# Kernel tuning notes

Measured on AMD Instinct MI355X. Metric: run time of the kernel, lower is better.

## Reference

```python
import jax, jax.numpy as jnp
import numpy as np

ALPHA = 0.2        # LeakyReLU negative slope (self.alpha)
NEG = -9e15        # mask value used by the torch module


def gru_cell(x, h, W_ih, W_hh, b_ih, b_hh):
    """torch.nn.GRUCell math. x, h: [N, F]; W_*: [3F, F]; b_*: [3F]. Gate order r,z,n."""
    gi = x @ W_ih.T + b_ih
    gh = h @ W_hh.T + b_hh
    ir, iz, i_n = jnp.split(gi, 3, axis=-1)
    hr, hz, h_n = jnp.split(gh, 3, axis=-1)
    r = jax.nn.sigmoid(ir + hr)
    z = jax.nn.sigmoid(iz + hz)
    n = jnp.tanh(i_n + r * h_n)
    return (1.0 - z) * n + z * h


def setup_inputs() -> dict:
    key = jax.random.key(0)
    N, F = 8192, 256
    ks = jax.random.split(key, 8)
    inputs = jax.random.normal(ks[0], (N, F), jnp.float32)
    # GRUCell parameters
    W_ih = jax.random.normal(ks[1], (3 * F, F), jnp.float32) / np.sqrt(F)
    W_hh = jax.random.normal(ks[2], (3 * F, F), jnp.float32) / np.sqrt(F)
    b_ih = jax.random.normal(ks[3], (3 * F,), jnp.float32) * 0.01
    b_hh = jax.random.normal(ks[4], (3 * F,), jnp.float32) * 0.01
    # GAT attention vector a: [2F, 1]
    a = jax.random.normal(ks[5], (2 * F, 1), jnp.float32) / np.sqrt(2.0 * F)
    # per-node neighbor pair (encodes weight_dict's 1-/2-neighbor cases)
    nbr = jax.random.randint(ks[6], (N, 2), 0, N)
    # dense adjacency, values in {0,1}
    adj = jax.random.randint(ks[7], (N, N), 0, 2).astype(jnp.int32)
    return dict(inputs=inputs, W_ih=W_ih, W_hh=W_hh, b_ih=b_ih, b_hh=b_hh,
                a=a, nbr=nbr, adj=adj)


def reference(inputs, W_ih, W_hh, b_ih, b_hh, a, nbr, adj):
    F_dim = inputs.shape[1]
    # per-node GRU aggregation: hidden = neighbor1 feature, input = neighbor2 feature
    h = inputs[nbr[:, 0]]                      # [N, F]
    x = inputs[nbr[:, 1]]                      # [N, F]
    outs = gru_cell(x, h, W_ih, W_hh, b_ih, b_hh)  # [N, F]
    # GAT scores: e[i,j] = leakyrelu([outs_i || outs_j] . a) = leakyrelu(f1_i + f2_j)
    # (decomposed -- avoids materializing the [N*N, 2F] concat of the original)
    a1 = a[:F_dim, 0]                          # [F]
    a2 = a[F_dim:, 0]                          # [F]
    e = jax.nn.leaky_relu((outs @ a1)[:, None] + (outs @ a2)[None, :], ALPHA)  # [N, N]
    e = jnp.where(adj > 0, e, NEG)
    return jax.nn.softmax(e, axis=1)
```

## Files before the change

### kernel.cpp

```cpp
#include <hip/hip_runtime.h>
#include <hip/hip_bf16.h>

#define NN 8192
#define FF 256
#define NEGV -9000000000000000.0f

typedef __bf16 bf16x8 __attribute__((ext_vector_type(8)));
typedef float f32x4 __attribute__((ext_vector_type(4)));
typedef int i32x4 __attribute__((ext_vector_type(4)));

__device__ __forceinline__ void load_lds16(const void* g, void* l) {
  auto gp = (const __attribute__((address_space(1))) void*)(uintptr_t)g;
  auto lp = (__attribute__((address_space(3))) void*)(uint32_t)(uintptr_t)l;
  __builtin_amdgcn_global_load_lds(gp, lp, 16, 0, 0);
}

__global__ __launch_bounds__(256) void k_convert(const float* __restrict__ inputs,
                                                 const float* __restrict__ Wih,
                                                 const float* __restrict__ Whh,
                                                 __hip_bfloat16* __restrict__ ibf,
                                                 __hip_bfloat16* __restrict__ Wc) {
  const int gid = blockIdx.x * 256 + threadIdx.x;
  const float* src;
  __hip_bfloat16* dst;
  if (gid < 262144) {
    src = inputs + (size_t)gid * 8;
    dst = ibf + (size_t)gid * 8;
  } else {
    const int o = gid - 262144;
    const int l = o & 63;
    const int ks = (o >> 6) & 7;
    const int w = (o >> 9) & 3;
    const int fbb = (o >> 11) & 3;
    const int g = o >> 13;
    const int row = g * 256 + fbb * 64 + w * 16 + (l & 15);
    const int col = (l >> 4) * 8 + ks * 32;
    src = (row < 768) ? (Wih + (size_t)row * FF + col)
                      : (Whh + (size_t)(row - 768) * FF + col);
    dst = Wc + (size_t)o * 8;
  }
  const float4 v0 = *(const float4*)src;
  const float4 v1 = *(const float4*)(src + 4);
  union { __hip_bfloat16 h[8]; uint4 u; } t;
  t.h[0] = __float2bfloat16(v0.x); t.h[1] = __float2bfloat16(v0.y);
  t.h[2] = __float2bfloat16(v0.z); t.h[3] = __float2bfloat16(v0.w);
  t.h[4] = __float2bfloat16(v1.x); t.h[5] = __float2bfloat16(v1.y);
  t.h[6] = __float2bfloat16(v1.z); t.h[7] = __float2bfloat16(v1.w);
  *(uint4*)dst = t.u;
}

__global__ __launch_bounds__(256) void k_gru(const __hip_bfloat16* __restrict__ ibf,
                                             const __hip_bfloat16* __restrict__ Wpk,
                                             const float* __restrict__ inputs,
                                             const int* __restrict__ nbr,
                                             const float* __restrict__ b_ih,
                                             const float* __restrict__ b_hh,
                                             const float* __restrict__ a,
                                             float* __restrict__ p1a,
                                             float* __restrict__ p2a) {
  __shared__ __align__(16) __hip_bfloat16 Ax[16 * 256];
  __shared__ __align__(16) __hip_bfloat16 Ah[16 * 256];
  __shared__ int hrow_s[16];
  __shared__ float r1[4][16], r2[4][16];
  const int rb = blockIdx.x * 16;
  const int fb = blockIdx.y;
  const int tid = threadIdx.x;
  const int w = tid >> 6, l = tid & 63;
  const int fl = l & 15, q = l >> 4;

  if (tid < 16) hrow_s[tid] = nbr[2 * (rb + tid)];

#pragma unroll
  for (int j = 0; j < 2; ++j) {
    const int r = w * 4 + j * 2 + (l >> 5);
    const int cs = l & 31;
    const int gc = cs ^ (r & 7);
    const int xr = nbr[2 * (rb + r) + 1];
    const int hr_ = nbr[2 * (rb + r)];
    load_lds16((const char*)(ibf + (size_t)xr * FF) + gc * 16,
               (char*)Ax + (w * 4 + j * 2) * 512);
    load_lds16((const char*)(ibf + (size_t)hr_ * FF) + gc * 16,
               (char*)Ah + (w * 4 + j * 2) * 512);
  }
  __syncthreads();

  const int f = fb * 64 + w * 16 + fl;
  const float bir = b_ih[f], biz = b_ih[256 + f], bin_ = b_ih[512 + f];
  const float bhr = b_hh[f], bhz = b_hh[256 + f], bhn = b_hh[512 + f];
  const float a1f = a[f], a2f = a[256 + f];

  f32x4 acc[6];
#pragma unroll
  for (int g = 0; g < 6; ++g) acc[g] = (f32x4){0, 0, 0, 0};

  bf16x8 axf[8], ahf[8];
#pragma unroll
  for (int ks = 0; ks < 8; ++ks) {
    const int c = ks * 4 + q;
    axf[ks] = *(const bf16x8*)((const char*)Ax + fl * 512 + (c ^ (fl & 7)) * 16);
    ahf[ks] = *(const bf16x8*)((const char*)Ah + fl * 512 + (c ^ (fl & 7)) * 16);
  }
#pragma unroll
  for (int g = 0; g < 3; ++g) {
    const int bi = ((g * 16 + fb * 4 + w) * 8) * 64 + l;
    const int bh = (((3 + g) * 16 + fb * 4 + w) * 8) * 64 + l;
#pragma unroll
    for (int ks = 0; ks < 8; ++ks) {
      const bf16x8 bfi = *(const bf16x8*)(Wpk + (size_t)(bi + ks * 64) * 8);
      const bf16x8 bfh = *(const bf16x8*)(Wpk + (size_t)(bh + ks * 64) * 8);
      acc[g]     = __builtin_amdgcn_mfma_f32_16x16x32_bf16(axf[ks], bfi, acc[g], 0, 0, 0);
      acc[3 + g] = __builtin_amdgcn_mfma_f32_16x16x32_bf16(ahf[ks], bfh, acc[3 + g], 0, 0, 0);
    }
  }

  float p1[4], p2[4];
#pragma unroll
  for (int j = 0; j < 4; ++j) {
    const int row = q * 4 + j;
    const float ir = acc[0][j] + bir;
    const float iz = acc[1][j] + biz;
    const float in_ = acc[2][j] + bin_;
    const float hrv = acc[3][j] + bhr;
    const float hzv = acc[4][j] + bhz;
    const float hnv = acc[5][j] + bhn;
    const float r_ = 1.f / (1.f + __expf(-(ir + hrv)));
    const float z_ = 1.f / (1.f + __expf(-(iz + hzv)));
    const float n_ = tanhf(in_ + r_ * hnv);
    const float hval = inputs[(size_t)hrow_s[row] * FF + f];
    const float o = (1.f - z_) * n_ + z_ * hval;
    p1[j] = o * a1f;
    p2[j] = o * a2f;
  }

#pragma unroll
  for (int j = 0; j < 4; ++j) {
#pragma unroll
    for (int off = 1; off < 16; off <<= 1) {
      p1[j] += __shfl_xor(p1[j], off);
      p2[j] += __shfl_xor(p2[j], off);
    }
  }
  if (fl == 0) {
#pragma unroll
    for (int j = 0; j < 4; ++j) {
      r1[w][q * 4 + j] = p1[j];
      r2[w][q * 4 + j] = p2[j];
    }
  }
  __syncthreads();
  if (tid < 16) {
    p1a[fb * NN + rb + tid] = r1[0][tid] + r1[1][tid] + r1[2][tid] + r1[3][tid];
  } else if (tid < 32) {
    const int t2 = tid - 16;
    p2a[fb * NN + rb + t2] = r2[0][t2] + r2[1][t2] + r2[2][t2] + r2[3][t2];
  }
}

__global__ __launch_bounds__(256) void k_reduce(const float* __restrict__ p1a,
                                                const float* __restrict__ p2a,
                                                float* __restrict__ s1,
                                                float* __restrict__ s2) {
  const int i = blockIdx.x * 256 + threadIdx.x;
  s1[i] = p1a[i] + p1a[NN + i] + p1a[2 * NN + i] + p1a[3 * NN + i];
  s2[i] = p2a[i] + p2a[NN + i] + p2a[2 * NN + i] + p2a[3 * NN + i];
}

__global__ __launch_bounds__(256, 5) void k_softmax(const int* __restrict__ adj,
                                                    const float* __restrict__ s1,
                                                    const float* __restrict__ s2,
                                                    float* __restrict__ out) {
  __shared__ float red[4];
  const int row = blockIdx.x;
  const int t = threadIdx.x;
  const i32x4* adjv = (const i32x4*)(adj + (size_t)row * NN);
  i32x4 a4[8];
#pragma unroll
  for (int k = 0; k < 8; ++k) a4[k] = __builtin_nontemporal_load(adjv + k * 256 + t);
  f32x4 sv[8];
#pragma unroll
  for (int k = 0; k < 8; ++k) sv[k] = *(const f32x4*)(s2 + (k * 256 + t) * 4);
  const float s1v = s1[row];

  float tsum = 0.f;
#pragma unroll
  for (int k = 0; k < 8; ++k) {
#pragma unroll
    for (int c = 0; c < 4; ++c) {
      float x = s1v + sv[k][c];
      x = (x > 0.f) ? x : 0.2f * x;
      x = (a4[k][c] > 0) ? x : NEGV;
      tsum += __expf(x);
    }
  }
#pragma unroll
  for (int off = 32; off; off >>= 1) tsum += __shfl_xor(tsum, off);
  if ((t & 63) == 0) red[t >> 6] = tsum;
  __syncthreads();
  const float inv = 1.f / (red[0] + red[1] + red[2] + red[3]);
  float* orow = out + (size_t)row * NN;
#pragma unroll
  for (int k = 0; k < 8; ++k) {
    const int v = k * 256 + t;
    f32x4 o;
#pragma unroll
    for (int c = 0; c < 4; ++c) {
      float x = s1v + sv[k][c];
      x = (x > 0.f) ? x : 0.2f * x;
      x = (a4[k][c] > 0) ? x : NEGV;
      o[c] = __expf(x) * inv;
    }
    __builtin_nontemporal_store(o, (f32x4*)(orow + v * 4));
  }
}

extern "C" void kernel_launch(void* const* d_in, const int* in_sizes, int n_in,
                              void* d_out, int out_size, void* d_ws, size_t ws_size,
                              hipStream_t stream) {
  const float* inputs = (const float*)d_in[0];
  const float* W_ih   = (const float*)d_in[1];
  const float* W_hh   = (const float*)d_in[2];
  const float* b_ih   = (const float*)d_in[3];
  const float* b_hh   = (const float*)d_in[4];
  const float* a      = (const float*)d_in[5];
  const int*   nbr    = (const int*)d_in[6];
  const int*   adj    = (const int*)d_in[7];
  float* out = (float*)d_out;

  __hip_bfloat16* ibf = (__hip_bfloat16*)((char*)d_out + (64u << 20));
  __hip_bfloat16* Wpk = (__hip_bfloat16*)((char*)d_out + (80u << 20));
  float* p1a = (float*)((char*)d_out + (96u << 20));
  float* p2a = p1a + 4 * NN;
  float* s1 = (float*)d_ws;
  float* s2 = s1 + NN;

  k_convert<<<1216, 256, 0, stream>>>(inputs, W_ih, W_hh, ibf, Wpk);
  k_gru<<<dim3(512, 4), 256, 0, stream>>>(ibf, Wpk, inputs, nbr, b_ih, b_hh, a, p1a, p2a);
  k_reduce<<<32, 256, 0, stream>>>(p1a, p2a, s1, s2);
  k_softmax<<<NN, 256, 0, stream>>>(adj, s1, s2, out);
}
```

Baseline: 123.3 us.

## Process eight softmax rows per block with double-buffered adjacency prefetch

The softmax kernel now handles eight consecutive rows per block instead of one. The s2 vector is loaded once per block and reused across those rows. The next row's adjacency is prefetched into registers while the current row is reduced and written, so load latency overlaps with compute. The cost is higher register pressure (two sets of adjacency registers, and the occupancy hint is removed) and a grid of 1024 blocks, which may leave fewer waves per CU to hide memory latency.

```diff
diff --git a/kernel.cpp b/kernel.cpp
--- a/kernel.cpp
+++ b/kernel.cpp
@@ -165,51 +165,62 @@
   s2[i] = p2a[i] + p2a[NN + i] + p2a[2 * NN + i] + p2a[3 * NN + i];
 }
 
-__global__ __launch_bounds__(256, 5) void k_softmax(const int* __restrict__ adj,
-                                                    const float* __restrict__ s1,
-                                                    const float* __restrict__ s2,
-                                                    float* __restrict__ out) {
-  __shared__ float red[4];
-  const int row = blockIdx.x;
+__global__ __launch_bounds__(256) void k_softmax(const int* __restrict__ adj,
+                                                 const float* __restrict__ s1,
+                                                 const float* __restrict__ s2,
+                                                 float* __restrict__ out) {
+  __shared__ float red[2][4];
   const int t = threadIdx.x;
-  const i32x4* adjv = (const i32x4*)(adj + (size_t)row * NN);
-  i32x4 a4[8];
-#pragma unroll
-  for (int k = 0; k < 8; ++k) a4[k] = __builtin_nontemporal_load(adjv + k * 256 + t);
   f32x4 sv[8];
 #pragma unroll
   for (int k = 0; k < 8; ++k) sv[k] = *(const f32x4*)(s2 + (k * 256 + t) * 4);
-  const float s1v = s1[row];
-
-  float tsum = 0.f;
-#pragma unroll
-  for (int k = 0; k < 8; ++k) {
-#pragma unroll
-    for (int c = 0; c < 4; ++c) {
-      float x = s1v + sv[k][c];
-      x = (x > 0.f) ? x : 0.2f * x;
-      x = (a4[k][c] > 0) ? x : NEGV;
-      tsum += __expf(x);
-    }
-  }
-#pragma unroll
-  for (int off = 32; off; off >>= 1) tsum += __shfl_xor(tsum, off);
-  if ((t & 63) == 0) red[t >> 6] = tsum;
-  __syncthreads();
-  const float inv = 1.f / (red[0] + red[1] + red[2] + red[3]);
-  float* orow = out + (size_t)row * NN;
-#pragma unroll
-  for (int k = 0; k < 8; ++k) {
-    const int v = k * 256 + t;
-    f32x4 o;
-#pragma unroll
-    for (int c = 0; c < 4; ++c) {
-      float x = s1v + sv[k][c];
-      x = (x > 0.f) ? x : 0.2f * x;
-      x = (a4[k][c] > 0) ? x : NEGV;
-      o[c] = __expf(x) * inv;
-    }
-    __builtin_nontemporal_store(o, (f32x4*)(orow + v * 4));
+
+  int row = blockIdx.x * 8;
+  i32x4 a4[8], b4[8];
+  const i32x4* adjv0 = (const i32x4*)(adj + (size_t)row * NN);
+#pragma unroll
+  for (int k = 0; k < 8; ++k) a4[k] = __builtin_nontemporal_load(adjv0 + k * 256 + t);
+
+  for (int it = 0; it < 8; ++it) {
+    if (it < 7) {
+      const i32x4* adjn = (const i32x4*)(adj + (size_t)(row + 1) * NN);
+#pragma unroll
+      for (int k = 0; k < 8; ++k) b4[k] = __builtin_nontemporal_load(adjn + k * 256 + t);
+    }
+    const float s1v = s1[row];
+
+    float tsum = 0.f;
+#pragma unroll
+    for (int k = 0; k < 8; ++k) {
+#pragma unroll
+      for (int c = 0; c < 4; ++c) {
+        float x = s1v + sv[k][c];
+        x = (x > 0.f) ? x : 0.2f * x;
+        x = (a4[k][c] > 0) ? x : NEGV;
+        tsum += __expf(x);
+      }
+    }
+#pragma unroll
+    for (int off = 32; off; off >>= 1) tsum += __shfl_xor(tsum, off);
+    if ((t & 63) == 0) red[it & 1][t >> 6] = tsum;
+    __syncthreads();
+    const float inv = 1.f / (red[it & 1][0] + red[it & 1][1] + red[it & 1][2] + red[it & 1][3]);
+    float* orow = out + (size_t)row * NN;
+#pragma unroll
+    for (int k = 0; k < 8; ++k) {
+      f32x4 o;
+#pragma unroll
+      for (int c = 0; c < 4; ++c) {
+        float x = s1v + sv[k][c];
+        x = (x > 0.f) ? x : 0.2f * x;
+        x = (a4[k][c] > 0) ? x : NEGV;
+        o[c] = __expf(x) * inv;
+      }
+      __builtin_nontemporal_store(o, (f32x4*)(orow + (k * 256 + t) * 4));
+    }
+#pragma unroll
+    for (int k = 0; k < 8; ++k) a4[k] = b4[k];
+    ++row;
   }
 }
 
@@ -236,5 +247,5 @@
   k_convert<<<1216, 256, 0, stream>>>(inputs, W_ih, W_hh, ibf, Wpk);
   k_gru<<<dim3(512, 4), 256, 0, stream>>>(ibf, Wpk, inputs, nbr, b_ih, b_hh, a, p1a, p2a);
   k_reduce<<<32, 256, 0, stream>>>(p1a, p2a, s1, s2);
-  k_softmax<<<NN, 256, 0, stream>>>(adj, s1, s2, out);
-}
+  k_softmax<<<1024, 256, 0, stream>>>(adj, s1, s2, out);
+}
```

Result: slower. 131.7 us (+6.8%).

## Fuse input bf16 conversion into GRU gather; cut softmax registers via bitmask

Applied to the files above, without the earlier changes.

The separate pass that converted all node features to bf16 is removed. The GRU kernel now gathers fp32 neighbor rows directly, converts them in registers and writes them swizzled into LDS, so the only pre-pass left packs the weights. The softmax kernel no longer keeps all adj and s2 vectors live. It packs the adjacency test into a 32-bit mask, reloads s2 in the second pass, and raises the occupancy hint to 8 blocks. In exchange, the gather moves twice the bytes per row, goes through registers instead of async global-to-LDS loads, and repeats the conversion across the 4 feature blocks.

```diff
diff --git a/kernel.cpp b/kernel.cpp
--- a/kernel.cpp
+++ b/kernel.cpp
@@ -9,36 +9,19 @@
 typedef float f32x4 __attribute__((ext_vector_type(4)));
 typedef int i32x4 __attribute__((ext_vector_type(4)));
 
-__device__ __forceinline__ void load_lds16(const void* g, void* l) {
-  auto gp = (const __attribute__((address_space(1))) void*)(uintptr_t)g;
-  auto lp = (__attribute__((address_space(3))) void*)(uint32_t)(uintptr_t)l;
-  __builtin_amdgcn_global_load_lds(gp, lp, 16, 0, 0);
-}
-
-__global__ __launch_bounds__(256) void k_convert(const float* __restrict__ inputs,
-                                                 const float* __restrict__ Wih,
-                                                 const float* __restrict__ Whh,
-                                                 __hip_bfloat16* __restrict__ ibf,
-                                                 __hip_bfloat16* __restrict__ Wc) {
-  const int gid = blockIdx.x * 256 + threadIdx.x;
-  const float* src;
-  __hip_bfloat16* dst;
-  if (gid < 262144) {
-    src = inputs + (size_t)gid * 8;
-    dst = ibf + (size_t)gid * 8;
-  } else {
-    const int o = gid - 262144;
-    const int l = o & 63;
-    const int ks = (o >> 6) & 7;
-    const int w = (o >> 9) & 3;
-    const int fbb = (o >> 11) & 3;
-    const int g = o >> 13;
-    const int row = g * 256 + fbb * 64 + w * 16 + (l & 15);
-    const int col = (l >> 4) * 8 + ks * 32;
-    src = (row < 768) ? (Wih + (size_t)row * FF + col)
-                      : (Whh + (size_t)(row - 768) * FF + col);
-    dst = Wc + (size_t)o * 8;
-  }
+__global__ __launch_bounds__(256) void k_pack(const float* __restrict__ Wih,
+                                              const float* __restrict__ Whh,
+                                              __hip_bfloat16* __restrict__ Wc) {
+  const int o = blockIdx.x * 256 + threadIdx.x;
+  const int l = o & 63;
+  const int ks = (o >> 6) & 7;
+  const int w = (o >> 9) & 3;
+  const int fbb = (o >> 11) & 3;
+  const int g = o >> 13;
+  const int row = g * 256 + fbb * 64 + w * 16 + (l & 15);
+  const int col = (l >> 4) * 8 + ks * 32;
+  const float* src = (row < 768) ? (Wih + (size_t)row * FF + col)
+                                 : (Whh + (size_t)(row - 768) * FF + col);
   const float4 v0 = *(const float4*)src;
   const float4 v1 = *(const float4*)(src + 4);
   union { __hip_bfloat16 h[8]; uint4 u; } t;
@@ -46,11 +29,10 @@
   t.h[2] = __float2bfloat16(v0.z); t.h[3] = __float2bfloat16(v0.w);
   t.h[4] = __float2bfloat16(v1.x); t.h[5] = __float2bfloat16(v1.y);
   t.h[6] = __float2bfloat16(v1.z); t.h[7] = __float2bfloat16(v1.w);
-  *(uint4*)dst = t.u;
-}
-
-__global__ __launch_bounds__(256) void k_gru(const __hip_bfloat16* __restrict__ ibf,
-                                             const __hip_bfloat16* __restrict__ Wpk,
+  *(uint4*)(Wc + (size_t)o * 8) = t.u;
+}
+
+__global__ __launch_bounds__(256) void k_gru(const __hip_bfloat16* __restrict__ Wpk,
                                              const float* __restrict__ inputs,
                                              const int* __restrict__ nbr,
                                              const float* __restrict__ b_ih,
@@ -73,14 +55,24 @@
 #pragma unroll
   for (int j = 0; j < 2; ++j) {
     const int r = w * 4 + j * 2 + (l >> 5);
-    const int cs = l & 31;
-    const int gc = cs ^ (r & 7);
+    const int gc = l & 31;
     const int xr = nbr[2 * (rb + r) + 1];
     const int hr_ = nbr[2 * (rb + r)];
-    load_lds16((const char*)(ibf + (size_t)xr * FF) + gc * 16,
-               (char*)Ax + (w * 4 + j * 2) * 512);
-    load_lds16((const char*)(ibf + (size_t)hr_ * FF) + gc * 16,
-               (char*)Ah + (w * 4 + j * 2) * 512);
+    const float4 xv0 = *(const float4*)(inputs + (size_t)xr * FF + gc * 8);
+    const float4 xv1 = *(const float4*)(inputs + (size_t)xr * FF + gc * 8 + 4);
+    const float4 hv0 = *(const float4*)(inputs + (size_t)hr_ * FF + gc * 8);
+    const float4 hv1 = *(const float4*)(inputs + (size_t)hr_ * FF + gc * 8 + 4);
+    union { __hip_bfloat16 hh[8]; uint4 u; } tx, th;
+    tx.hh[0] = __float2bfloat16(xv0.x); tx.hh[1] = __float2bfloat16(xv0.y);
+    tx.hh[2] = __float2bfloat16(xv0.z); tx.hh[3] = __float2bfloat16(xv0.w);
+    tx.hh[4] = __float2bfloat16(xv1.x); tx.hh[5] = __float2bfloat16(xv1.y);
+    tx.hh[6] = __float2bfloat16(xv1.z); tx.hh[7] = __float2bfloat16(xv1.w);
+    th.hh[0] = __float2bfloat16(hv0.x); th.hh[1] = __float2bfloat16(hv0.y);
+    th.hh[2] = __float2bfloat16(hv0.z); th.hh[3] = __float2bfloat16(hv0.w);
+    th.hh[4] = __float2bfloat16(hv1.x); th.hh[5] = __float2bfloat16(hv1.y);
+    th.hh[6] = __float2bfloat16(hv1.z); th.hh[7] = __float2bfloat16(hv1.w);
+    *(uint4*)((char*)Ax + r * 512 + (gc ^ (r & 7)) * 16) = tx.u;
+    *(uint4*)((char*)Ah + r * 512 + (gc ^ (r & 7)) * 16) = th.u;
   }
   __syncthreads();
 
@@ -165,7 +157,7 @@
   s2[i] = p2a[i] + p2a[NN + i] + p2a[2 * NN + i] + p2a[3 * NN + i];
 }
 
-__global__ __launch_bounds__(256, 5) void k_softmax(const int* __restrict__ adj,
+__global__ __launch_bounds__(256, 8) void k_softmax(const int* __restrict__ adj,
                                                     const float* __restrict__ s1,
                                                     const float* __restrict__ s2,
                                                     float* __restrict__ out) {
@@ -173,22 +165,21 @@
   const int row = blockIdx.x;
   const int t = threadIdx.x;
   const i32x4* adjv = (const i32x4*)(adj + (size_t)row * NN);
-  i32x4 a4[8];
-#pragma unroll
-  for (int k = 0; k < 8; ++k) a4[k] = __builtin_nontemporal_load(adjv + k * 256 + t);
-  f32x4 sv[8];
-#pragma unroll
-  for (int k = 0; k < 8; ++k) sv[k] = *(const f32x4*)(s2 + (k * 256 + t) * 4);
   const float s1v = s1[row];
 
+  unsigned mask = 0u;
   float tsum = 0.f;
 #pragma unroll
   for (int k = 0; k < 8; ++k) {
+    const i32x4 a4 = __builtin_nontemporal_load(adjv + k * 256 + t);
+    const f32x4 sv = *(const f32x4*)(s2 + (k * 256 + t) * 4);
 #pragma unroll
     for (int c = 0; c < 4; ++c) {
-      float x = s1v + sv[k][c];
+      float x = s1v + sv[c];
       x = (x > 0.f) ? x : 0.2f * x;
-      x = (a4[k][c] > 0) ? x : NEGV;
+      const bool on = a4[c] > 0;
+      mask |= (on ? 1u : 0u) << (k * 4 + c);
+      x = on ? x : NEGV;
       tsum += __expf(x);
     }
   }
@@ -200,16 +191,16 @@
   float* orow = out + (size_t)row * NN;
 #pragma unroll
   for (int k = 0; k < 8; ++k) {
-    const int v = k * 256 + t;
+    const f32x4 sv = *(const f32x4*)(s2 + (k * 256 + t) * 4);
     f32x4 o;
 #pragma unroll
     for (int c = 0; c < 4; ++c) {
-      float x = s1v + sv[k][c];
+      float x = s1v + sv[c];
       x = (x > 0.f) ? x : 0.2f * x;
-      x = (a4[k][c] > 0) ? x : NEGV;
+      x = ((mask >> (k * 4 + c)) & 1u) ? x : NEGV;
       o[c] = __expf(x) * inv;
     }
-    __builtin_nontemporal_store(o, (f32x4*)(orow + v * 4));
+    __builtin_nontemporal_store(o, (f32x4*)(orow + (k * 256 + t) * 4));
   }
 }
 
@@ -226,15 +217,14 @@
   const int*   adj    = (const int*)d_in[7];
   float* out = (float*)d_out;
 
-  __hip_bfloat16* ibf = (__hip_bfloat16*)((char*)d_out + (64u << 20));
   __hip_bfloat16* Wpk = (__hip_bfloat16*)((char*)d_out + (80u << 20));
   float* p1a = (float*)((char*)d_out + (96u << 20));
   float* p2a = p1a + 4 * NN;
   float* s1 = (float*)d_ws;
   float* s2 = s1 + NN;
 
-  k_convert<<<1216, 256, 0, stream>>>(inputs, W_ih, W_hh, ibf, Wpk);
-  k_gru<<<dim3(512, 4), 256, 0, stream>>>(ibf, Wpk, inputs, nbr, b_ih, b_hh, a, p1a, p2a);
+  k_pack<<<192, 256, 0, stream>>>(W_ih, W_hh, Wpk);
+  k_gru<<<dim3(512, 4), 256, 0, stream>>>(Wpk, inputs, nbr, b_ih, b_hh, a, p1a, p2a);
   k_reduce<<<32, 256, 0, stream>>>(p1a, p2a, s1, s2);
   k_softmax<<<NN, 256, 0, stream>>>(adj, s1, s2, out);
 }
```

Measured after the change: 135.1 us. +9.5%, slower.
